# Kernel optimization log

Measured on AMD Instinct MI355X. Metric: run time of the kernel, lower is better.

Reference implementation:

```python
import jax, jax.numpy as jnp
import numpy as np

N = 100000
DEG = 16
E = N * DEG
F = 256
U = 128


def setup_inputs() -> dict:
    key = jax.random.key(0)
    k1, k2, k3, k4, k5 = jax.random.split(key, 5)
    node_states = jax.random.normal(k1, (1, N, F), dtype=jnp.float32)
    # edges[:,0] must be sorted ascending for the repeat/bincount softmax trick
    src = jnp.repeat(jnp.arange(N, dtype=jnp.int32), DEG)
    dst = jax.random.randint(k2, (E,), 0, N, dtype=jnp.int32)
    edges = jnp.stack([src, dst], axis=-1)[None]  # [1, E, 2]
    edge_weights = jax.random.uniform(k3, (1, E), dtype=jnp.float32)
    kernel = jax.random.normal(k4, (F, U), dtype=jnp.float32) * (1.0 / np.sqrt(F))
    kernel_attention = jax.random.normal(k5, (2 * U, 1), dtype=jnp.float32) * 0.05
    return {"node_states": node_states, "edges": edges,
            "edge_weights": edge_weights, "kernel": kernel,
            "kernel_attention": kernel_attention}


def reference(node_states, edges, edge_weights, kernel, kernel_attention):
    ns = node_states[0]          # [N, F]
    e = edges[0]                 # [E, 2], src sorted
    ew = edge_weights[0]         # [E]
    n_nodes = ns.shape[0]

    h = ns @ kernel                                   # [N, U]
    pair = h[e].reshape(e.shape[0], -1)               # gather -> [E, 2U]
    pair = pair * ew[:, None]
    scores = jax.nn.leaky_relu(pair @ kernel_attention,
                               negative_slope=0.2)[:, 0]   # tf default alpha=0.2
    scores = jnp.exp(jnp.clip(scores, -2.0, 2.0))
    ssum = jax.ops.segment_sum(scores, e[:, 0], num_segments=n_nodes)  # [N]
    # edges[:,0] sorted => repeat(ssum, bincount) == ssum[e[:,0]]
    norm = scores / ssum[e[:, 0]]
    out = jax.ops.segment_sum(h[e[:, 1]] * norm[:, None], e[:, 0],
                              num_segments=n_nodes)   # [N, U]
    return out
```

## Files before the change

### kernel.cpp

```cpp
#include <hip/hip_runtime.h>
#include <hip/hip_bf16.h>
#include <cstdint>

#define NN 100000
#define DEG 16
#define FF 256
#define UU 128

typedef __attribute__((ext_vector_type(8))) short short8;
typedef __attribute__((ext_vector_type(4))) float f32x4;

__device__ __forceinline__ unsigned short f2bf(float x) {
    uint32_t u = __builtin_bit_cast(uint32_t, x);
    uint32_t r = (u + 0x7fffu + ((u >> 16) & 1u)) >> 16;
    return (unsigned short)r;
}
__device__ __forceinline__ float bf2f(unsigned short b) {
    return __builtin_bit_cast(float, (uint32_t)b << 16);
}
__device__ __forceinline__ uint32_t cvt_pk_bf16(float lo, float hi) {
    uint32_t r;
    asm("v_cvt_pk_bf16_f32 %0, %1, %2" : "=v"(r) : "v"(lo), "v"(hi));
    return r;
}

#define GLL16(gp, lp) __builtin_amdgcn_global_load_lds( \
    (const __attribute__((address_space(1))) void*)(gp), \
    (__attribute__((address_space(3))) void*)(lp), 16, 0, 0)

__global__ void k_convW(const float* __restrict__ W, unsigned short* __restrict__ Wt) {
    int i = blockIdx.x * 256 + threadIdx.x;
    int k = i >> 7, c = i & 127;
    Wt[c * 256 + k] = f2bf(W[i]);
}

__global__ __launch_bounds__(256, 3) void k_gemm(
    const float* __restrict__ ns, const unsigned short* __restrict__ Wt,
    const float* __restrict__ ka, unsigned short* __restrict__ hb,
    float* __restrict__ a_src, float* __restrict__ a_dst)
{
    __shared__ char smem[32 * 1024 + 1024];
    float* ka_s = (float*)(smem + 32768);
    const int t = threadIdx.x;
    const int lane = t & 63;
    const int w = t >> 6;
    const int row0 = blockIdx.x * 32;
    const int lrow = lane & 15;
    const int khalf = lane >> 4;

    ka_s[t] = ka[t];

    short8 bfrag[2][8];
    {
        const int col0 = w * 32 + lrow;
        #pragma unroll
        for (int nt = 0; nt < 2; ++nt) {
            const unsigned short* wp = Wt + (size_t)(col0 + nt * 16) * 256 + khalf * 8;
            #pragma unroll
            for (int ks = 0; ks < 8; ++ks)
                bfrag[nt][ks] = *(const short8*)(wp + ks * 32);
        }
    }
    #pragma unroll
    for (int nt = 0; nt < 2; ++nt)
        #pragma unroll
        for (int ks = 0; ks < 8; ++ks)
            asm volatile("" : "+v"(bfrag[nt][ks]));

    #pragma unroll
    for (int i = 0; i < 8; ++i) {
        const int r = w * 8 + i;
        const float* src = ns + (size_t)(row0 + r) * FF + ((lane ^ (r & 7)) * 4);
        GLL16(src, smem + r * 1024);
    }
    __syncthreads();

    f32x4 acc[2][2];
    #pragma unroll
    for (int mt = 0; mt < 2; ++mt)
        #pragma unroll
        for (int nt = 0; nt < 2; ++nt)
            acc[mt][nt] = (f32x4){0.f, 0.f, 0.f, 0.f};

    #pragma unroll
    for (int ks = 0; ks < 8; ++ks) {
        short8 a[2];
        #pragma unroll
        for (int mt = 0; mt < 2; ++mt) {
            const int row = mt * 16 + lrow;
            const int kg = ks * 8 + khalf * 2;
            const char* rb = smem + row * 1024;
            f32x4 x0 = *(const f32x4*)(rb + ((kg ^ (row & 7)) * 16));
            f32x4 x1 = *(const f32x4*)(rb + (((kg + 1) ^ (row & 7)) * 16));
            uint4 u;
            u.x = cvt_pk_bf16(x0[0], x0[1]);
            u.y = cvt_pk_bf16(x0[2], x0[3]);
            u.z = cvt_pk_bf16(x1[0], x1[1]);
            u.w = cvt_pk_bf16(x1[2], x1[3]);
            a[mt] = __builtin_bit_cast(short8, u);
        }
        #pragma unroll
        for (int mt = 0; mt < 2; ++mt)
            #pragma unroll
            for (int nt = 0; nt < 2; ++nt)
                acc[mt][nt] = __builtin_amdgcn_mfma_f32_16x16x32_bf16(
                    a[mt], bfrag[nt][ks], acc[mt][nt], 0, 0, 0);
    }

    __syncthreads();

    unsigned short* Hs = (unsigned short*)smem;
    {
        const int wcol = w * 32;
        #pragma unroll
        for (int mt = 0; mt < 2; ++mt)
            #pragma unroll
            for (int nt = 0; nt < 2; ++nt)
                #pragma unroll
                for (int r = 0; r < 4; ++r) {
                    int row = mt * 16 + khalf * 4 + r;
                    int col = wcol + nt * 16 + lrow;
                    Hs[row * 136 + col] = f2bf(acc[mt][nt][r]);
                }
    }
    __syncthreads();

    {
        const int row = t >> 3, q8 = t & 7;
        const int gr = row0 + row;
        short8 hv0 = *(const short8*)(Hs + row * 136 + q8 * 16);
        short8 hv1 = *(const short8*)(Hs + row * 136 + q8 * 16 + 8);
        float ps = 0.f, pd = 0.f;
        #pragma unroll
        for (int e = 0; e < 8; ++e) {
            int c = q8 * 16 + e;
            ps = fmaf(bf2f((unsigned short)hv0[e]), ka_s[c], ps);
            pd = fmaf(bf2f((unsigned short)hv0[e]), ka_s[UU + c], pd);
            ps = fmaf(bf2f((unsigned short)hv1[e]), ka_s[c + 8], ps);
            pd = fmaf(bf2f((unsigned short)hv1[e]), ka_s[UU + c + 8], pd);
        }
        short8* op = (short8*)(hb + (size_t)gr * UU + q8 * 16);
        op[0] = hv0;
        op[1] = hv1;
        ps += __shfl_xor(ps, 1, 64); ps += __shfl_xor(ps, 2, 64); ps += __shfl_xor(ps, 4, 64);
        pd += __shfl_xor(pd, 1, 64); pd += __shfl_xor(pd, 2, 64); pd += __shfl_xor(pd, 4, 64);
        if (q8 == 0) { a_src[gr] = ps; a_dst[gr] = pd; }
    }
}

__global__ __launch_bounds__(256, 8) void k_edge(
    const int* __restrict__ edges, const float* __restrict__ ew,
    const float* __restrict__ a_src, const float* __restrict__ a_dst,
    uint32_t* __restrict__ nd)
{
    const int ei = blockIdx.x * 256 + threadIdx.x;
    const int n = ei >> 4;
    const int dst = edges[2 * ei + 1];
    const float w = ew[ei];
    const float x0 = w * (a_src[n] + a_dst[dst]);
    float x = x0 > 0.f ? x0 : 0.2f * x0;
    x = fminf(2.f, fmaxf(-2.f, x));
    const float s = __expf(x);

    float ssum = s;
    ssum += __shfl_xor(ssum, 1, 64);
    ssum += __shfl_xor(ssum, 2, 64);
    ssum += __shfl_xor(ssum, 4, 64);
    ssum += __shfl_xor(ssum, 8, 64);
    const float norm = s / ssum;

    uint32_t q15 = (uint32_t)(norm * 32768.f + 0.5f);
    if (q15 > 32767u) q15 = 32767u;
    nd[ei] = ((uint32_t)dst << 15) | q15;
}

__global__ __launch_bounds__(256, 4) void k_agg(
    const uint32_t* __restrict__ nd, const unsigned short* __restrict__ hb,
    float* __restrict__ out)
{
    const int t = threadIdx.x;
    const int lane = t & 63;
    const int wv = t >> 6;
    const int g = lane >> 4;
    const int q = lane & 15;
    const int n = blockIdx.x * 16 + wv * 4 + g;

    const uint32_t v = nd[(size_t)n * DEG + q];
    const uint32_t dstB = (v >> 15) << 8;
    const float normf = (float)(v & 32767u) * (1.f / 32768.f);
    const int gb = lane & 48;

    uint32_t ab[16];
    #pragma unroll
    for (int j = 0; j < 16; ++j) ab[j] = __shfl(dstB, gb | j, 64);

    const char* hbase = (const char*)hb + q * 16;
    uint4 r[16];
    #pragma unroll
    for (int j = 0; j < 16; ++j) r[j] = *(const uint4*)(hbase + ab[j]);

    float nf[16];
    #pragma unroll
    for (int j = 0; j < 16; ++j) nf[j] = __shfl(normf, gb | j, 64);

    float acc[8];
    #pragma unroll
    for (int d = 0; d < 8; ++d) acc[d] = 0.f;
    #pragma unroll
    for (int j = 0; j < 16; ++j) {
        acc[0] = fmaf(nf[j], __builtin_bit_cast(float, r[j].x << 16), acc[0]);
        acc[1] = fmaf(nf[j], __builtin_bit_cast(float, r[j].x & 0xffff0000u), acc[1]);
        acc[2] = fmaf(nf[j], __builtin_bit_cast(float, r[j].y << 16), acc[2]);
        acc[3] = fmaf(nf[j], __builtin_bit_cast(float, r[j].y & 0xffff0000u), acc[3]);
        acc[4] = fmaf(nf[j], __builtin_bit_cast(float, r[j].z << 16), acc[4]);
        acc[5] = fmaf(nf[j], __builtin_bit_cast(float, r[j].z & 0xffff0000u), acc[5]);
        acc[6] = fmaf(nf[j], __builtin_bit_cast(float, r[j].w << 16), acc[6]);
        acc[7] = fmaf(nf[j], __builtin_bit_cast(float, r[j].w & 0xffff0000u), acc[7]);
    }

    float* op = out + (size_t)n * UU + q * 8;
    float4 o0, o1;
    o0.x = acc[0]; o0.y = acc[1]; o0.z = acc[2]; o0.w = acc[3];
    o1.x = acc[4]; o1.y = acc[5]; o1.z = acc[6]; o1.w = acc[7];
    *(float4*)op = o0;
    *(float4*)(op + 4) = o1;
}

extern "C" void kernel_launch(void* const* d_in, const int* in_sizes, int n_in,
                              void* d_out, int out_size, void* d_ws, size_t ws_size,
                              hipStream_t stream) {
    const float* ns    = (const float*)d_in[0];
    const int*   edges = (const int*)d_in[1];
    const float* ew    = (const float*)d_in[2];
    const float* W     = (const float*)d_in[3];
    const float* ka    = (const float*)d_in[4];
    float* out = (float*)d_out;

    char* ws = (char*)d_ws;
    unsigned short* hb = (unsigned short*)ws;
    float* a_src = (float*)(ws + (size_t)NN * UU * 2);
    float* a_dst = a_src + NN;
    unsigned short* Wt = (unsigned short*)(ws + (size_t)NN * UU * 2 + 2 * (size_t)NN * 4);
    uint32_t* nd = (uint32_t*)(ws + (size_t)NN * UU * 2 + 2 * (size_t)NN * 4 + 65536);

    k_convW<<<FF * UU / 256, 256, 0, stream>>>(W, Wt);
    k_gemm<<<NN / 32, 256, 0, stream>>>(ns, Wt, ka, hb, a_src, a_dst);
    k_edge<<<NN * DEG / 256, 256, 0, stream>>>(edges, ew, a_src, a_dst, nd);
    k_agg<<<NN / 16, 256, 0, stream>>>(nd, hb, out);
}
```

Before: 112.6 us.

## Load GEMM A operands directly to registers with prefetch; pin gather loads

The GEMM kernel no longer stages the fp32 node-state tile in LDS through global_load_lds. Each lane now reads its A-fragment values straight from global memory into registers, prefetching the next k-step while the current one feeds the MFMAs. This removes a barrier and cuts LDS use, which may allow more blocks per CU, but the per-lane global reads are strided 32-byte accesses with less coalescing. In the aggregation kernel, an empty asm barrier forces all 16 gathered rows to be loaded before the FMA loop starts, so the loads are issued together.

Result: slower. 149.9 us (+33.1%).

```diff
diff --git a/kernel.cpp b/kernel.cpp
--- a/kernel.cpp
+++ b/kernel.cpp
@@ -9,6 +9,7 @@
 
 typedef __attribute__((ext_vector_type(8))) short short8;
 typedef __attribute__((ext_vector_type(4))) float f32x4;
+typedef __attribute__((ext_vector_type(4))) unsigned int u32x4;
 
 __device__ __forceinline__ unsigned short f2bf(float x) {
     uint32_t u = __builtin_bit_cast(uint32_t, x);
@@ -23,10 +24,6 @@
     asm("v_cvt_pk_bf16_f32 %0, %1, %2" : "=v"(r) : "v"(lo), "v"(hi));
     return r;
 }
-
-#define GLL16(gp, lp) __builtin_amdgcn_global_load_lds( \
-    (const __attribute__((address_space(1))) void*)(gp), \
-    (__attribute__((address_space(3))) void*)(lp), 16, 0, 0)
 
 __global__ void k_convW(const float* __restrict__ W, unsigned short* __restrict__ Wt) {
     int i = blockIdx.x * 256 + threadIdx.x;
@@ -39,8 +36,8 @@
     const float* __restrict__ ka, unsigned short* __restrict__ hb,
     float* __restrict__ a_src, float* __restrict__ a_dst)
 {
-    __shared__ char smem[32 * 1024 + 1024];
-    float* ka_s = (float*)(smem + 32768);
+    __shared__ char smem[32 * 136 * 2 + 1024];
+    float* ka_s = (float*)(smem + 32 * 136 * 2);
     const int t = threadIdx.x;
     const int lane = t & 63;
     const int w = t >> 6;
@@ -67,13 +64,10 @@
         for (int ks = 0; ks < 8; ++ks)
             asm volatile("" : "+v"(bfrag[nt][ks]));
 
-    #pragma unroll
-    for (int i = 0; i < 8; ++i) {
-        const int r = w * 8 + i;
-        const float* src = ns + (size_t)(row0 + r) * FF + ((lane ^ (r & 7)) * 4);
-        GLL16(src, smem + r * 1024);
-    }
-    __syncthreads();
+    const float* arow[2];
+    #pragma unroll
+    for (int mt = 0; mt < 2; ++mt)
+        arow[mt] = ns + (size_t)(row0 + mt * 16 + lrow) * FF + khalf * 8;
 
     f32x4 acc[2][2];
     #pragma unroll
@@ -82,21 +76,29 @@
         for (int nt = 0; nt < 2; ++nt)
             acc[mt][nt] = (f32x4){0.f, 0.f, 0.f, 0.f};
 
+    f32x4 c0[2], c1[2], n0[2], n1[2];
+    #pragma unroll
+    for (int mt = 0; mt < 2; ++mt) {
+        c0[mt] = *(const f32x4*)(arow[mt]);
+        c1[mt] = *(const f32x4*)(arow[mt] + 4);
+    }
     #pragma unroll
     for (int ks = 0; ks < 8; ++ks) {
+        if (ks < 7) {
+            #pragma unroll
+            for (int mt = 0; mt < 2; ++mt) {
+                n0[mt] = *(const f32x4*)(arow[mt] + (ks + 1) * 32);
+                n1[mt] = *(const f32x4*)(arow[mt] + (ks + 1) * 32 + 4);
+            }
+        }
         short8 a[2];
         #pragma unroll
         for (int mt = 0; mt < 2; ++mt) {
-            const int row = mt * 16 + lrow;
-            const int kg = ks * 8 + khalf * 2;
-            const char* rb = smem + row * 1024;
-            f32x4 x0 = *(const f32x4*)(rb + ((kg ^ (row & 7)) * 16));
-            f32x4 x1 = *(const f32x4*)(rb + (((kg + 1) ^ (row & 7)) * 16));
-            uint4 u;
-            u.x = cvt_pk_bf16(x0[0], x0[1]);
-            u.y = cvt_pk_bf16(x0[2], x0[3]);
-            u.z = cvt_pk_bf16(x1[0], x1[1]);
-            u.w = cvt_pk_bf16(x1[2], x1[3]);
+            u32x4 u;
+            u[0] = cvt_pk_bf16(c0[mt][0], c0[mt][1]);
+            u[1] = cvt_pk_bf16(c0[mt][2], c0[mt][3]);
+            u[2] = cvt_pk_bf16(c1[mt][0], c1[mt][1]);
+            u[3] = cvt_pk_bf16(c1[mt][2], c1[mt][3]);
             a[mt] = __builtin_bit_cast(short8, u);
         }
         #pragma unroll
@@ -105,9 +107,9 @@
             for (int nt = 0; nt < 2; ++nt)
                 acc[mt][nt] = __builtin_amdgcn_mfma_f32_16x16x32_bf16(
                     a[mt], bfrag[nt][ks], acc[mt][nt], 0, 0, 0);
-    }
-
-    __syncthreads();
+        #pragma unroll
+        for (int mt = 0; mt < 2; ++mt) { c0[mt] = n0[mt]; c1[mt] = n1[mt]; }
+    }
 
     unsigned short* Hs = (unsigned short*)smem;
     {
@@ -195,27 +197,30 @@
     for (int j = 0; j < 16; ++j) ab[j] = __shfl(dstB, gb | j, 64);
 
     const char* hbase = (const char*)hb + q * 16;
-    uint4 r[16];
-    #pragma unroll
-    for (int j = 0; j < 16; ++j) r[j] = *(const uint4*)(hbase + ab[j]);
+    u32x4 r[16];
+    #pragma unroll
+    for (int j = 0; j < 16; ++j) r[j] = *(const u32x4*)(hbase + ab[j]);
 
     float nf[16];
     #pragma unroll
     for (int j = 0; j < 16; ++j) nf[j] = __shfl(normf, gb | j, 64);
 
+    #pragma unroll
+    for (int j = 0; j < 16; ++j) asm volatile("" : "+v"(r[j]));
+
     float acc[8];
     #pragma unroll
     for (int d = 0; d < 8; ++d) acc[d] = 0.f;
     #pragma unroll
     for (int j = 0; j < 16; ++j) {
-        acc[0] = fmaf(nf[j], __builtin_bit_cast(float, r[j].x << 16), acc[0]);
-        acc[1] = fmaf(nf[j], __builtin_bit_cast(float, r[j].x & 0xffff0000u), acc[1]);
-        acc[2] = fmaf(nf[j], __builtin_bit_cast(float, r[j].y << 16), acc[2]);
-        acc[3] = fmaf(nf[j], __builtin_bit_cast(float, r[j].y & 0xffff0000u), acc[3]);
-        acc[4] = fmaf(nf[j], __builtin_bit_cast(float, r[j].z << 16), acc[4]);
-        acc[5] = fmaf(nf[j], __builtin_bit_cast(float, r[j].z & 0xffff0000u), acc[5]);
-        acc[6] = fmaf(nf[j], __builtin_bit_cast(float, r[j].w << 16), acc[6]);
-        acc[7] = fmaf(nf[j], __builtin_bit_cast(float, r[j].w & 0xffff0000u), acc[7]);
+        acc[0] = fmaf(nf[j], __builtin_bit_cast(float, r[j][0] << 16), acc[0]);
+        acc[1] = fmaf(nf[j], __builtin_bit_cast(float, r[j][0] & 0xffff0000u), acc[1]);
+        acc[2] = fmaf(nf[j], __builtin_bit_cast(float, r[j][1] << 16), acc[2]);
+        acc[3] = fmaf(nf[j], __builtin_bit_cast(float, r[j][1] & 0xffff0000u), acc[3]);
+        acc[4] = fmaf(nf[j], __builtin_bit_cast(float, r[j][2] << 16), acc[4]);
+        acc[5] = fmaf(nf[j], __builtin_bit_cast(float, r[j][2] & 0xffff0000u), acc[5]);
+        acc[6] = fmaf(nf[j], __builtin_bit_cast(float, r[j][3] << 16), acc[6]);
+        acc[7] = fmaf(nf[j], __builtin_bit_cast(float, r[j][3] & 0xffff0000u), acc[7]);
     }
 
     float* op = out + (size_t)n * UU + q * 8;
```

## Slice h by column groups for cache-local aggregation and persist GEMM with double buffering

Applied to the files above, without the earlier changes.

The projected features h are now stored as eight column slices of 16 bf16 values each (3.2 MB per slice). The aggregation kernel runs slice-major, so each block gathers only 32-byte rows from one slice, which is meant to keep the gathered data resident in L2/LLC instead of doing random 256-byte gathers over the full 25.6 MB array. The GEMM becomes a persistent kernel with 512 blocks that double-buffers input tiles in LDS through global_load_lds, overlapping the loads with MFMA work. The cost is more edge-index reloads (each nd entry is read once per slice), extra shuffle reductions, and more LDS per block, which lowers GEMM occupancy.

After: 162.3 us. +44.1%, slower.

```diff
diff --git a/kernel.cpp b/kernel.cpp
--- a/kernel.cpp
+++ b/kernel.cpp
@@ -6,9 +6,15 @@
 #define DEG 16
 #define FF 256
 #define UU 128
+#define SLICE_BYTES 3200000
+#define NTILE 3125
+#define GEMM_BLOCKS 512
 
 typedef __attribute__((ext_vector_type(8))) short short8;
 typedef __attribute__((ext_vector_type(4))) float f32x4;
+typedef __attribute__((ext_vector_type(4))) unsigned int u32x4;
+
+#define PIN8(a,b,c,d,e,f,g,h) asm volatile("" : "+v"(a),"+v"(b),"+v"(c),"+v"(d),"+v"(e),"+v"(f),"+v"(g),"+v"(h))
 
 __device__ __forceinline__ unsigned short f2bf(float x) {
     uint32_t u = __builtin_bit_cast(uint32_t, x);
@@ -23,7 +29,6 @@
     asm("v_cvt_pk_bf16_f32 %0, %1, %2" : "=v"(r) : "v"(lo), "v"(hi));
     return r;
 }
-
 #define GLL16(gp, lp) __builtin_amdgcn_global_load_lds( \
     (const __attribute__((address_space(1))) void*)(gp), \
     (__attribute__((address_space(3))) void*)(lp), 16, 0, 0)
@@ -34,17 +39,17 @@
     Wt[c * 256 + k] = f2bf(W[i]);
 }
 
-__global__ __launch_bounds__(256, 3) void k_gemm(
+__global__ __launch_bounds__(256, 2) void k_gemm(
     const float* __restrict__ ns, const unsigned short* __restrict__ Wt,
-    const float* __restrict__ ka, unsigned short* __restrict__ hb,
+    const float* __restrict__ ka, unsigned short* __restrict__ hbs,
     float* __restrict__ a_src, float* __restrict__ a_dst)
 {
-    __shared__ char smem[32 * 1024 + 1024];
-    float* ka_s = (float*)(smem + 32768);
+    __shared__ char smem[2 * 32768 + 32 * 136 * 2 + 1024];
+    unsigned short* Hs = (unsigned short*)(smem + 65536);
+    float* ka_s = (float*)(smem + 65536 + 8704);
     const int t = threadIdx.x;
     const int lane = t & 63;
     const int w = t >> 6;
-    const int row0 = blockIdx.x * 32;
     const int lrow = lane & 15;
     const int khalf = lane >> 4;
 
@@ -61,90 +66,104 @@
                 bfrag[nt][ks] = *(const short8*)(wp + ks * 32);
         }
     }
-    #pragma unroll
-    for (int nt = 0; nt < 2; ++nt)
-        #pragma unroll
-        for (int ks = 0; ks < 8; ++ks)
-            asm volatile("" : "+v"(bfrag[nt][ks]));
-
-    #pragma unroll
-    for (int i = 0; i < 8; ++i) {
-        const int r = w * 8 + i;
-        const float* src = ns + (size_t)(row0 + r) * FF + ((lane ^ (r & 7)) * 4);
-        GLL16(src, smem + r * 1024);
-    }
-    __syncthreads();
-
-    f32x4 acc[2][2];
-    #pragma unroll
-    for (int mt = 0; mt < 2; ++mt)
-        #pragma unroll
-        for (int nt = 0; nt < 2; ++nt)
-            acc[mt][nt] = (f32x4){0.f, 0.f, 0.f, 0.f};
-
-    #pragma unroll
-    for (int ks = 0; ks < 8; ++ks) {
-        short8 a[2];
-        #pragma unroll
-        for (int mt = 0; mt < 2; ++mt) {
-            const int row = mt * 16 + lrow;
-            const int kg = ks * 8 + khalf * 2;
-            const char* rb = smem + row * 1024;
-            f32x4 x0 = *(const f32x4*)(rb + ((kg ^ (row & 7)) * 16));
-            f32x4 x1 = *(const f32x4*)(rb + (((kg + 1) ^ (row & 7)) * 16));
-            uint4 u;
-            u.x = cvt_pk_bf16(x0[0], x0[1]);
-            u.y = cvt_pk_bf16(x0[2], x0[3]);
-            u.z = cvt_pk_bf16(x1[0], x1[1]);
-            u.w = cvt_pk_bf16(x1[2], x1[3]);
-            a[mt] = __builtin_bit_cast(short8, u);
-        }
+    PIN8(bfrag[0][0], bfrag[0][1], bfrag[0][2], bfrag[0][3],
+         bfrag[0][4], bfrag[0][5], bfrag[0][6], bfrag[0][7]);
+    PIN8(bfrag[1][0], bfrag[1][1], bfrag[1][2], bfrag[1][3],
+         bfrag[1][4], bfrag[1][5], bfrag[1][6], bfrag[1][7]);
+
+    auto stage = [&](int tile, char* buf) {
+        #pragma unroll
+        for (int i = 0; i < 8; ++i) {
+            const int rr = w * 8 + i;
+            const float* src = ns + (size_t)(tile * 32 + rr) * FF + ((lane ^ (rr & 7)) * 4);
+            GLL16(src, buf + rr * 1024);
+        }
+    };
+
+    int cur = 0;
+    stage(blockIdx.x, smem);
+
+    for (int tl = blockIdx.x; tl < NTILE; tl += GEMM_BLOCKS) {
+        asm volatile("s_waitcnt vmcnt(0) lgkmcnt(0)" ::: "memory");
+        __builtin_amdgcn_sched_barrier(0);
+        __builtin_amdgcn_s_barrier();
+
+        const int nxt = tl + GEMM_BLOCKS;
+        if (nxt < NTILE) stage(nxt, smem + (cur ^ 1) * 32768);
+        __builtin_amdgcn_sched_barrier(0);
+
+        const char* buf = smem + cur * 32768;
+        f32x4 acc[2][2];
         #pragma unroll
         for (int mt = 0; mt < 2; ++mt)
             #pragma unroll
             for (int nt = 0; nt < 2; ++nt)
-                acc[mt][nt] = __builtin_amdgcn_mfma_f32_16x16x32_bf16(
-                    a[mt], bfrag[nt][ks], acc[mt][nt], 0, 0, 0);
-    }
-
-    __syncthreads();
-
-    unsigned short* Hs = (unsigned short*)smem;
-    {
-        const int wcol = w * 32;
-        #pragma unroll
-        for (int mt = 0; mt < 2; ++mt)
-            #pragma unroll
-            for (int nt = 0; nt < 2; ++nt)
+                acc[mt][nt] = (f32x4){0.f, 0.f, 0.f, 0.f};
+
+        #pragma unroll
+        for (int ks = 0; ks < 8; ++ks) {
+            short8 a[2];
+            #pragma unroll
+            for (int mt = 0; mt < 2; ++mt) {
+                const int row = mt * 16 + lrow;
+                const int kg = ks * 8 + khalf * 2;
+                const char* rb = buf + row * 1024;
+                f32x4 x0 = *(const f32x4*)(rb + ((kg ^ (row & 7)) * 16));
+                f32x4 x1 = *(const f32x4*)(rb + (((kg + 1) ^ (row & 7)) * 16));
+                u32x4 u;
+                u[0] = cvt_pk_bf16(x0[0], x0[1]);
+                u[1] = cvt_pk_bf16(x0[2], x0[3]);
+                u[2] = cvt_pk_bf16(x1[0], x1[1]);
+                u[3] = cvt_pk_bf16(x1[2], x1[3]);
+                a[mt] = __builtin_bit_cast(short8, u);
+            }
+            #pragma unroll
+            for (int mt = 0; mt < 2; ++mt)
                 #pragma unroll
-                for (int r = 0; r < 4; ++r) {
-                    int row = mt * 16 + khalf * 4 + r;
-                    int col = wcol + nt * 16 + lrow;
-                    Hs[row * 136 + col] = f2bf(acc[mt][nt][r]);
-                }
-    }
-    __syncthreads();
-
-    {
-        const int row = t >> 3, q8 = t & 7;
-        const int gr = row0 + row;
-        short8 hv0 = *(const short8*)(Hs + row * 136 + q8 * 16);
-        short8 hv1 = *(const short8*)(Hs + row * 136 + q8 * 16 + 8);
-        float ps = 0.f, pd = 0.f;
-        #pragma unroll
-        for (int e = 0; e < 8; ++e) {
-            int c = q8 * 16 + e;
-            ps = fmaf(bf2f((unsigned short)hv0[e]), ka_s[c], ps);
-            pd = fmaf(bf2f((unsigned short)hv0[e]), ka_s[UU + c], pd);
-            ps = fmaf(bf2f((unsigned short)hv1[e]), ka_s[c + 8], ps);
-            pd = fmaf(bf2f((unsigned short)hv1[e]), ka_s[UU + c + 8], pd);
-        }
-        short8* op = (short8*)(hb + (size_t)gr * UU + q8 * 16);
-        op[0] = hv0;
-        op[1] = hv1;
-        ps += __shfl_xor(ps, 1, 64); ps += __shfl_xor(ps, 2, 64); ps += __shfl_xor(ps, 4, 64);
-        pd += __shfl_xor(pd, 1, 64); pd += __shfl_xor(pd, 2, 64); pd += __shfl_xor(pd, 4, 64);
-        if (q8 == 0) { a_src[gr] = ps; a_dst[gr] = pd; }
+                for (int nt = 0; nt < 2; ++nt)
+                    acc[mt][nt] = __builtin_amdgcn_mfma_f32_16x16x32_bf16(
+                        a[mt], bfrag[nt][ks], acc[mt][nt], 0, 0, 0);
+        }
+
+        {
+            const int wcol = w * 32;
+            #pragma unroll
+            for (int mt = 0; mt < 2; ++mt)
+                #pragma unroll
+                for (int nt = 0; nt < 2; ++nt)
+                    #pragma unroll
+                    for (int r = 0; r < 4; ++r) {
+                        int row = mt * 16 + khalf * 4 + r;
+                        int col = wcol + nt * 16 + lrow;
+                        Hs[row * 136 + col] = f2bf(acc[mt][nt][r]);
+                    }
+        }
+        asm volatile("s_waitcnt lgkmcnt(0)" ::: "memory");
+        __builtin_amdgcn_sched_barrier(0);
+        __builtin_amdgcn_s_barrier();
+
+        {
+            const int row = t >> 3, q8 = t & 7;
+            const int gr = tl * 32 + row;
+            short8 hv0 = *(const short8*)(Hs + row * 136 + q8 * 16);
+            short8 hv1 = *(const short8*)(Hs + row * 136 + q8 * 16 + 8);
+            float ps = 0.f, pd = 0.f;
+            #pragma unroll
+            for (int e = 0; e < 8; ++e) {
+                int c = q8 * 16 + e;
+                ps = fmaf(bf2f((unsigned short)hv0[e]), ka_s[c], ps);
+                pd = fmaf(bf2f((unsigned short)hv0[e]), ka_s[UU + c], pd);
+                ps = fmaf(bf2f((unsigned short)hv1[e]), ka_s[c + 8], ps);
+                pd = fmaf(bf2f((unsigned short)hv1[e]), ka_s[UU + c + 8], pd);
+            }
+            char* base = (char*)hbs + (size_t)q8 * SLICE_BYTES + (size_t)gr * 32;
+            *(short8*)(base) = hv0;
+            *(short8*)(base + 16) = hv1;
+            ps += __shfl_xor(ps, 1, 64); ps += __shfl_xor(ps, 2, 64); ps += __shfl_xor(ps, 4, 64);
+            pd += __shfl_xor(pd, 1, 64); pd += __shfl_xor(pd, 2, 64); pd += __shfl_xor(pd, 4, 64);
+            if (q8 == 0) { a_src[gr] = ps; a_dst[gr] = pd; }
+        }
+        cur ^= 1;
     }
 }
 
@@ -174,56 +193,53 @@
     nd[ei] = ((uint32_t)dst << 15) | q15;
 }
 
-__global__ __launch_bounds__(256, 4) void k_agg(
-    const uint32_t* __restrict__ nd, const unsigned short* __restrict__ hb,
+__global__ __launch_bounds__(256, 8) void k_agg(
+    const uint32_t* __restrict__ nd, const unsigned short* __restrict__ hbs,
     float* __restrict__ out)
 {
     const int t = threadIdx.x;
-    const int lane = t & 63;
-    const int wv = t >> 6;
-    const int g = lane >> 4;
-    const int q = lane & 15;
-    const int n = blockIdx.x * 16 + wv * 4 + g;
-
-    const uint32_t v = nd[(size_t)n * DEG + q];
-    const uint32_t dstB = (v >> 15) << 8;
-    const float normf = (float)(v & 32767u) * (1.f / 32768.f);
-    const int gb = lane & 48;
-
-    uint32_t ab[16];
+    const int slice = blockIdx.x & 7;
+    const int nb = blockIdx.x >> 3;
+    const int nl = t >> 2;
+    const int q = t & 3;
+    const int n = nb * 64 + nl;
+    const bool valid = n < NN;
+    const int nc = valid ? n : NN - 1;
+
+    const u32x4 ndv = *(const u32x4*)(nd + (size_t)nc * DEG + q * 4);
+    const char* hs = (const char*)hbs + (size_t)slice * SLICE_BYTES;
+
+    float acc[16];
     #pragma unroll
-    for (int j = 0; j < 16; ++j) ab[j] = __shfl(dstB, gb | j, 64);
-
-    const char* hbase = (const char*)hb + q * 16;
-    uint4 r[16];
+    for (int d = 0; d < 16; ++d) acc[d] = 0.f;
+
     #pragma unroll
-    for (int j = 0; j < 16; ++j) r[j] = *(const uint4*)(hbase + ab[j]);
-
-    float nf[16];
+    for (int j = 0; j < 4; ++j) {
+        const uint32_t v = ndv[j];
+        const char* p = hs + ((size_t)(v >> 15) << 5);
+        const u32x4 r0 = *(const u32x4*)p;
+        const u32x4 r1 = *(const u32x4*)(p + 16);
+        const float nf = (float)(v & 32767u) * (1.f / 32768.f);
+        #pragma unroll
+        for (int d = 0; d < 4; ++d) {
+            acc[2 * d]     = fmaf(nf, __builtin_bit_cast(float, r0[d] << 16), acc[2 * d]);
+            acc[2 * d + 1] = fmaf(nf, __builtin_bit_cast(float, r0[d] & 0xffff0000u), acc[2 * d + 1]);
+            acc[8 + 2 * d]     = fmaf(nf, __builtin_bit_cast(float, r1[d] << 16), acc[8 + 2 * d]);
+            acc[8 + 2 * d + 1] = fmaf(nf, __builtin_bit_cast(float, r1[d] & 0xffff0000u), acc[8 + 2 * d + 1]);
+        }
+    }
+
     #pragma unroll
-    for (int j = 0; j < 16; ++j) nf[j] = __shfl(normf, gb | j, 64);
-
-    float acc[8];
-    #pragma unroll
-    for (int d = 0; d < 8; ++d) acc[d] = 0.f;
-    #pragma unroll
-    for (int j = 0; j < 16; ++j) {
-        acc[0] = fmaf(nf[j], __builtin_bit_cast(float, r[j].x << 16), acc[0]);
-        acc[1] = fmaf(nf[j], __builtin_bit_cast(float, r[j].x & 0xffff0000u), acc[1]);
-        acc[2] = fmaf(nf[j], __builtin_bit_cast(float, r[j].y << 16), acc[2]);
-        acc[3] = fmaf(nf[j], __builtin_bit_cast(float, r[j].y & 0xffff0000u), acc[3]);
-        acc[4] = fmaf(nf[j], __builtin_bit_cast(float, r[j].z << 16), acc[4]);
-        acc[5] = fmaf(nf[j], __builtin_bit_cast(float, r[j].z & 0xffff0000u), acc[5]);
-        acc[6] = fmaf(nf[j], __builtin_bit_cast(float, r[j].w << 16), acc[6]);
-        acc[7] = fmaf(nf[j], __builtin_bit_cast(float, r[j].w & 0xffff0000u), acc[7]);
-    }
-
-    float* op = out + (size_t)n * UU + q * 8;
-    float4 o0, o1;
-    o0.x = acc[0]; o0.y = acc[1]; o0.z = acc[2]; o0.w = acc[3];
-    o1.x = acc[4]; o1.y = acc[5]; o1.z = acc[6]; o1.w = acc[7];
-    *(float4*)op = o0;
-    *(float4*)(op + 4) = o1;
+    for (int d = 0; d < 16; ++d) {
+        acc[d] += __shfl_xor(acc[d], 1, 64);
+        acc[d] += __shfl_xor(acc[d], 2, 64);
+    }
+
+    if (valid) {
+        float4 o;
+        o.x = acc[q * 4]; o.y = acc[q * 4 + 1]; o.z = acc[q * 4 + 2]; o.w = acc[q * 4 + 3];
+        *(float4*)(out + (size_t)n * UU + slice * 16 + q * 4) = o;
+    }
 }
 
 extern "C" void kernel_launch(void* const* d_in, const int* in_sizes, int n_in,
@@ -237,14 +253,14 @@
     float* out = (float*)d_out;
 
     char* ws = (char*)d_ws;
-    unsigned short* hb = (unsigned short*)ws;
-    float* a_src = (float*)(ws + (size_t)NN * UU * 2);
+    unsigned short* hbs = (unsigned short*)ws;
+    float* a_src = (float*)(ws + (size_t)8 * SLICE_BYTES);
     float* a_dst = a_src + NN;
-    unsigned short* Wt = (unsigned short*)(ws + (size_t)NN * UU * 2 + 2 * (size_t)NN * 4);
-    uint32_t* nd = (uint32_t*)(ws + (size_t)NN * UU * 2 + 2 * (size_t)NN * 4 + 65536);
+    unsigned short* Wt = (unsigned short*)(ws + (size_t)8 * SLICE_BYTES + 2 * (size_t)NN * 4);
+    uint32_t* nd = (uint32_t*)(ws + (size_t)8 * SLICE_BYTES + 2 * (size_t)NN * 4 + 65536);
 
     k_convW<<<FF * UU / 256, 256, 0, stream>>>(W, Wt);
-    k_gemm<<<NN / 32, 256, 0, stream>>>(ns, Wt, ka, hb, a_src, a_dst);
+    k_gemm<<<GEMM_BLOCKS, 256, 0, stream>>>(ns, Wt, ka, hbs, a_src, a_dst);
     k_edge<<<NN * DEG / 256, 256, 0, stream>>>(edges, ew, a_src, a_dst, nd);
-    k_agg<<<NN / 16, 256, 0, stream>>>(nd, hb, out);
-}
+    k_agg<<<8 * 1563, 256, 0, stream>>>(nd, hbs, out);
+}
```
